# Performance work log

Measured on AMD Instinct MI355X. Metric: run time of the kernel, lower is better.

Reference implementation:

```python
import jax, jax.numpy as jnp
import numpy as np
import math

NLAT, NLON = 46, 90      # equiangular grid (in_shape == out_shape)
CH = 256                 # channels == kdim == vdim
BATCH = 1

def _cc_weights(n):
    # Clenshaw-Curtis quadrature weights (Waldvogel), nodes cos(k*pi/(n-1)); matches torch-harmonics equiangular grid
    n1 = n - 1
    N = np.arange(1, n1, 2)
    l = len(N)
    m = n1 - l
    v = np.concatenate([2.0 / N / (N - 2), [1.0 / N[-1]], np.zeros(m)])
    v = -v[:-1] - v[-1:0:-1]
    g0 = -np.ones(n1)
    g0[l] += n1
    g0[m] += n1
    g = g0 / (n1 ** 2 - 1 + (n1 % 2))
    w = np.fft.ifft(v + g).real
    return np.concatenate([w, w[:1]])

def _precompute_sparsity():
    # replicates _precompute_neighborhood_sparsity_s2: YZY-rotated north pole indicator within theta_cutoff
    lats = np.linspace(0.0, math.pi, NLAT)               # colatitudes of equiangular grid
    quad = (2.0 * math.pi / NLON) * _cc_weights(NLAT)    # per-latitude quadrature weights
    cutoff = math.pi / (NLAT - 1)                        # default theta_cutoff
    lons = np.linspace(0.0, 2.0 * math.pi, NLON + 1)[:-1]
    rows, cols = [], []
    for t in range(NLAT):
        a = -lats[t]
        beta = lons[None, :]
        gamma = lats[:, None]
        z = -np.cos(beta) * np.sin(a) * np.sin(gamma) + np.cos(a) * np.cos(gamma)
        x = np.cos(a) * np.cos(beta) * np.sin(gamma) + np.cos(gamma) * np.sin(a)
        y = np.sin(beta) * np.sin(gamma)
        nrm = np.sqrt(x * x + y * y + z * z)
        theta = np.arccos(np.clip(z / nrm, -1.0, 1.0))
        ii, jj = np.nonzero(theta <= cutoff)
        rows.append(np.full(ii.shape, t, dtype=np.int64))
        cols.append(ii * NLON + jj)
    row_ids = np.concatenate(rows).astype(np.int32)   # CSR row id per nnz (sorted)
    col_idx = np.concatenate(cols).astype(np.int32)   # flattened input index (at wo=0)
    return row_ids, col_idx, quad.astype(np.float32)

def setup_inputs() -> dict:
    key = jax.random.key(0)
    ks = jax.random.split(key, 9)
    row_ids, col_idx, quad = _precompute_sparsity()
    scale = 0.02  # sane init scale (module uses raw randn; trained weights would be O(this))
    return {
        "qo": jax.random.normal(ks[0], (BATCH, CH, NLAT, NLON), dtype=jnp.float32),
        "ki": jax.random.normal(ks[1], (BATCH, CH, NLAT, NLON), dtype=jnp.float32),
        "vi": jax.random.normal(ks[2], (BATCH, CH, NLAT, NLON), dtype=jnp.float32),
        "q_w": jax.random.normal(ks[3], (CH, CH), dtype=jnp.float32) * scale,
        "k_w": jax.random.normal(ks[4], (CH, CH), dtype=jnp.float32) * scale,
        "v_w": jax.random.normal(ks[5], (CH, CH), dtype=jnp.float32) * scale,
        "q_b": jax.random.normal(ks[6], (CH,), dtype=jnp.float32) * scale,
        "k_b": jax.random.normal(ks[7], (CH,), dtype=jnp.float32) * scale,
        "v_b": jax.random.normal(ks[8], (CH,), dtype=jnp.float32) * scale,
        "quad_w": jnp.asarray(quad),
        "row_ids": jnp.asarray(row_ids),
        "col_idx": jnp.asarray(col_idx),
    }

def reference(qo, ki, vi, q_w, k_w, v_w, q_b, k_b, v_b, quad_w, row_ids, col_idx):
    nlat, nlon = qo.shape[2], qo.shape[3]
    # 1x1 conv projections (F.conv2d with [out,in,1,1] kernels)
    q = jnp.einsum("kc,bchw->bkhw", q_w, qo) + q_b[None, :, None, None]
    k = jnp.einsum("kc,bchw->bkhw", k_w, ki) + k_b[None, :, None, None]
    v = jnp.einsum("vc,bchw->bvhw", v_w, vi) + v_b[None, :, None, None]

    hi = col_idx // nlon                                   # [N] input latitude per nnz
    wi0 = col_idx % nlon                                   # [N] input longitude at wo=0
    wo = jnp.arange(nlon)
    wi = (wi0[:, None] + wo[None, :]) % nlon               # [N, nlon] longitudes rotated by output lon

    kg = k[:, :, hi[:, None], wi]                          # [B, kdim, N, nlon] gathered keys
    qg = q[:, :, row_ids, :]                               # [B, kdim, N, nlon] query of owning output row
    qdotk = jnp.einsum("bcnw,bcnw->nbw", qg, kg)           # [N, B, nlon]

    # quadrature-weighted softmax over each output point's neighborhood (segment = output latitude row)
    seg_max = jax.ops.segment_max(qdotk, row_ids, num_segments=nlat, indices_are_sorted=True)
    seg_max = jax.lax.stop_gradient(seg_max)               # max shift cancels exactly in the ratio
    alpha = jnp.exp(qdotk - seg_max[row_ids]) * quad_w[hi][:, None, None]   # [N, B, nlon]
    denom = jax.ops.segment_sum(alpha, row_ids, num_segments=nlat, indices_are_sorted=True)  # [nlat, B, nlon]

    vg = jnp.transpose(v[:, :, hi[:, None], wi], (2, 0, 1, 3))   # [N, B, vdim, nlon]
    num = jax.ops.segment_sum(alpha[:, :, None, :] * vg, row_ids, num_segments=nlat, indices_are_sorted=True)
    out = num / denom[:, :, None, :]                       # [nlat, B, vdim, nlon]
    return jnp.transpose(out, (1, 2, 0, 3))                # [B, vdim, nlat, nlon]
```

## Files before the change

kernel.cpp:

```cpp
#include <hip/hip_runtime.h>
#include <math.h>

#define NLAT 46
#define NLON 90
#define CH   256
#define HW   (NLAT*NLON)
#define HWP  4160
#define HWT  32
#define NHT  130
#define XSTR 264

#define LIGHT_PER_XCD 473
#define SLOTS_PER_XCD (45 + LIGHT_PER_XCD)

typedef __attribute__((ext_vector_type(8))) short short8;
typedef __attribute__((ext_vector_type(4))) float floatx4;

__device__ __forceinline__ ushort f2bf(float f){
  uint u = __float_as_uint(f);
  u += 0x7fff + ((u >> 16) & 1);
  return (ushort)(u >> 16);
}
__device__ __forceinline__ float bf2f(ushort u){
  return __uint_as_float(((uint)u) << 16);
}

__device__ __forceinline__ int lower_bound_i(const int* __restrict__ a, int n, int key){
  int lo = 0, hi = n;
  while (lo < hi){ int mid = (lo + hi) >> 1; if (a[mid] < key) lo = mid + 1; else hi = mid; }
  return lo;
}

__global__ __launch_bounds__(256) void cast_w_kernel(
    const float* __restrict__ qw, const float* __restrict__ kw, const float* __restrict__ vw,
    ushort* __restrict__ Wq, ushort* __restrict__ Wk, ushort* __restrict__ Wv)
{
  const float* W; ushort* O;
  if (blockIdx.y == 0){ W = qw; O = Wq; }
  else if (blockIdx.y == 1){ W = kw; O = Wk; }
  else { W = vw; O = Wv; }
  for (int i = blockIdx.x * 256 + threadIdx.x; i < (CH*CH)/4; i += 8*256){
    float4 w = ((const float4*)W)[i];
    ushort4 o;
    o.x = f2bf(w.x); o.y = f2bf(w.y); o.z = f2bf(w.z); o.w = f2bf(w.w);
    ((ushort4*)O)[i] = o;
  }
}

__global__ __launch_bounds__(256) void fproj_kernel(
    const float* __restrict__ qo, const float* __restrict__ ki, const float* __restrict__ vi,
    const ushort* __restrict__ Wq, const ushort* __restrict__ Wk, const ushort* __restrict__ Wv,
    const float* __restrict__ qb, const float* __restrict__ kb, const float* __restrict__ vb,
    ushort* __restrict__ qP, ushort* __restrict__ kP, ushort* __restrict__ vP)
{
  const float* X; const ushort* Wb; const float* Bias; ushort* Out;
  if (blockIdx.y == 0){ X = qo; Wb = Wq; Bias = qb; Out = qP; }
  else if (blockIdx.y == 1){ X = ki; Wb = Wk; Bias = kb; Out = kP; }
  else { X = vi; Wb = Wv; Bias = vb; Out = vP; }

  __shared__ ushort Xs[HWT][XSTR];

  const int tid = threadIdx.x;
  const int hw0 = blockIdx.x * HWT;

  {
    int hwL = tid & 31;
    int cb  = tid >> 5;
    int hw  = hw0 + hwL;
    bool ok = hw < HW;
    const float* Xp = X + (size_t)(cb*32)*HW + (ok ? hw : 0);
    #pragma unroll
    for (int g = 0; g < 4; g++){
      short8 pk;
      #pragma unroll
      for (int u = 0; u < 8; u++){
        float f = ok ? Xp[(size_t)(g*8 + u)*HW] : 0.f;
        pk[u] = (short)f2bf(f);
      }
      *(short8*)(&Xs[hwL][cb*32 + g*8]) = pk;
    }
  }
  __syncthreads();

  const int lane = tid & 63;
  const int wave = tid >> 6;
  const int lm = lane & 15;
  const int lq = lane >> 4;
  const int kout_w = wave * 64;

  const ushort* Ap = Wb + (size_t)(kout_w + lm)*CH + lq*8;

  floatx4 acc[4][2];
  #pragma unroll
  for (int i = 0; i < 4; i++)
    #pragma unroll
    for (int j = 0; j < 2; j++) acc[i][j] = (floatx4){0,0,0,0};

  #pragma unroll
  for (int k0 = 0; k0 < 8; k0++){
    short8 a[4], b[2];
    #pragma unroll
    for (int i = 0; i < 4; i++)
      a[i] = *(const short8*)(Ap + (size_t)i*16*CH + k0*32);
    #pragma unroll
    for (int j = 0; j < 2; j++)
      b[j] = *(const short8*)(&Xs[j*16 + lm][lq*8 + k0*32]);
    #pragma unroll
    for (int i = 0; i < 4; i++)
      #pragma unroll
      for (int j = 0; j < 2; j++)
        acc[i][j] = __builtin_amdgcn_mfma_f32_16x16x32_bf16(a[i], b[j], acc[i][j], 0, 0, 0);
  }

  #pragma unroll
  for (int i = 0; i < 4; i++){
    int kout = kout_w + i*16 + lq*4;
    float4 bias = *(const float4*)(Bias + kout);
    #pragma unroll
    for (int j = 0; j < 2; j++){
      int hw = hw0 + j*16 + lm;
      if (hw < HW){
        ushort4 o;
        o.x = f2bf(acc[i][j][0] + bias.x);
        o.y = f2bf(acc[i][j][1] + bias.y);
        o.z = f2bf(acc[i][j][2] + bias.z);
        o.w = f2bf(acc[i][j][3] + bias.w);
        *(ushort4*)(Out + (size_t)hw*CH + kout) = o;
      }
    }
  }
}

__device__ __forceinline__ float4 ld_bf4(const ushort* p, int lane){
  ushort4 u = ((const ushort4*)p)[lane];
  float4 f;
  f.x = bf2f(u.x); f.y = bf2f(u.y); f.z = bf2f(u.z); f.w = bf2f(u.w);
  return f;
}

__global__ __launch_bounds__(256) void attn_kernel(
    const ushort* __restrict__ qP, const ushort* __restrict__ kP, const ushort* __restrict__ vP,
    const float* __restrict__ quad_w, const int* __restrict__ row_ids,
    const int* __restrict__ col_idx, int nnz, float* __restrict__ out)
{
  const int bid  = blockIdx.x;
  const int xcd  = bid & 7;
  const int slot = bid >> 3;

  int t, wo;
  if (slot < 45){
    int hu   = xcd * 45 + slot;
    int hidx = hu / 90;
    t  = (hidx < 2) ? hidx : 42 + hidx;
    wo = hu - hidx * 90;
  } else {
    int lu = xcd * LIGHT_PER_XCD + (slot - 45);
    if (lu >= 42 * NLON) return;
    int li = lu / NLON;
    t  = li + 2;
    wo = lu - li * NLON;
  }

  const int tid  = threadIdx.x;
  const int lane = tid & 63;
  const int wave = tid >> 6;

  const int start = lower_bound_i(row_ids, nnz, t);
  const int end   = lower_bound_i(row_ids, nnz, t + 1);

  const float4 qf = ld_bf4(qP + (size_t)(t * NLON + wo) * CH, lane);

  float denom = 0.f;
  float4 acc = make_float4(0.f, 0.f, 0.f, 0.f);

  int n = start + wave;
  for (; n + 4 < end; n += 8){
    int ciA = col_idx[n];
    int hiA = ciA / NLON;
    int wiA = ciA - hiA*NLON + wo; if (wiA >= NLON) wiA -= NLON;
    size_t offA = ((size_t)hiA*NLON + wiA) * CH;
    int ciB = col_idx[n + 4];
    int hiB = ciB / NLON;
    int wiB = ciB - hiB*NLON + wo; if (wiB >= NLON) wiB -= NLON;
    size_t offB = ((size_t)hiB*NLON + wiB) * CH;

    float4 kfA = ld_bf4(kP + offA, lane);
    float4 kfB = ld_bf4(kP + offB, lane);
    float sA = qf.x*kfA.x + qf.y*kfA.y + qf.z*kfA.z + qf.w*kfA.w;
    float sB = qf.x*kfB.x + qf.y*kfB.y + qf.z*kfB.z + qf.w*kfB.w;
    #pragma unroll
    for (int o = 32; o >= 1; o >>= 1){
      sA += __shfl_xor(sA, o, 64);
      sB += __shfl_xor(sB, o, 64);
    }
    float eA = __expf(sA) * quad_w[hiA];
    float eB = __expf(sB) * quad_w[hiB];
    float4 vfA = ld_bf4(vP + offA, lane);
    float4 vfB = ld_bf4(vP + offB, lane);
    denom += eA + eB;
    acc.x += eA*vfA.x + eB*vfB.x;
    acc.y += eA*vfA.y + eB*vfB.y;
    acc.z += eA*vfA.z + eB*vfB.z;
    acc.w += eA*vfA.w + eB*vfB.w;
  }
  if (n < end){
    int ci = col_idx[n];
    int hi = ci / NLON;
    int wi = ci - hi*NLON + wo; if (wi >= NLON) wi -= NLON;
    size_t off = ((size_t)hi*NLON + wi) * CH;
    float4 kf = ld_bf4(kP + off, lane);
    float s = qf.x*kf.x + qf.y*kf.y + qf.z*kf.z + qf.w*kf.w;
    #pragma unroll
    for (int o = 32; o >= 1; o >>= 1) s += __shfl_xor(s, o, 64);
    float e = __expf(s) * quad_w[hi];
    float4 vf = ld_bf4(vP + off, lane);
    denom += e;
    acc.x += e*vf.x; acc.y += e*vf.y; acc.z += e*vf.z; acc.w += e*vf.w;
  }

  __shared__ float sden[4];
  __shared__ float sacc[4][CH];
  if (lane == 0) sden[wave] = denom;
  sacc[wave][lane*4+0] = acc.x;
  sacc[wave][lane*4+1] = acc.y;
  sacc[wave][lane*4+2] = acc.z;
  sacc[wave][lane*4+3] = acc.w;
  __syncthreads();

  const float den = sden[0] + sden[1] + sden[2] + sden[3];
  const float num = sacc[0][tid] + sacc[1][tid] + sacc[2][tid] + sacc[3][tid];
  out[(size_t)tid * HW + t * NLON + wo] = num / den;
}

extern "C" void kernel_launch(void* const* d_in, const int* in_sizes, int n_in,
                              void* d_out, int out_size, void* d_ws, size_t ws_size,
                              hipStream_t stream)
{
  const float* qo   = (const float*)d_in[0];
  const float* ki   = (const float*)d_in[1];
  const float* vi   = (const float*)d_in[2];
  const float* qw   = (const float*)d_in[3];
  const float* kw   = (const float*)d_in[4];
  const float* vw   = (const float*)d_in[5];
  const float* qb   = (const float*)d_in[6];
  const float* kb   = (const float*)d_in[7];
  const float* vb   = (const float*)d_in[8];
  const float* quad = (const float*)d_in[9];
  const int* row_ids = (const int*)d_in[10];
  const int* col_idx = (const int*)d_in[11];
  const int nnz = in_sizes[10];

  ushort* ws = (ushort*)d_ws;
  const size_t TSZ = (size_t)HWP * CH;
  ushort* qP = ws;        ushort* kP = qP + TSZ;   ushort* vP = kP + TSZ;
  ushort* Wq = vP + TSZ;  ushort* Wk = Wq + CH*CH; ushort* Wv = Wk + CH*CH;

  cast_w_kernel<<<dim3(8, 3), 256, 0, stream>>>(qw, kw, vw, Wq, Wk, Wv);
  fproj_kernel<<<dim3(NHT, 3), 256, 0, stream>>>(qo, ki, vi, Wq, Wk, Wv, qb, kb, vb, qP, kP, vP);
  attn_kernel<<<dim3(8 * SLOTS_PER_XCD), 256, 0, stream>>>(qP, kP, vP, quad, row_ids, col_idx, nnz, (float*)d_out);
}
```

Measured before the change: 124.1 us.

## Fuse weight cast into projection and split attention waves into 16-lane groups

Drops the separate weight-cast kernel: the projection kernel now reads fp32 weights and converts them to bf16 in registers, which saves one launch but re-reads fp32 weights in every block. The attention kernel is restructured so each wave handles four neighbors at once, with each 16-lane group covering a full 256-channel row using 16-element vector loads. The dot-product reduction shrinks to a 4-step shuffle, and the cross-group accumulator reduction is deferred to the end. This raises register use per thread.

```diff
diff --git a/kernel.cpp b/kernel.cpp
--- a/kernel.cpp
+++ b/kernel.cpp
@@ -24,6 +24,9 @@
 __device__ __forceinline__ float bf2f(ushort u){
   return __uint_as_float(((uint)u) << 16);
 }
+__device__ __forceinline__ float bf2fs(short s){
+  return __uint_as_float(((uint)(ushort)s) << 16);
+}
 
 __device__ __forceinline__ int lower_bound_i(const int* __restrict__ a, int n, int key){
   int lo = 0, hi = n;
@@ -31,32 +34,16 @@
   return lo;
 }
 
-__global__ __launch_bounds__(256) void cast_w_kernel(
-    const float* __restrict__ qw, const float* __restrict__ kw, const float* __restrict__ vw,
-    ushort* __restrict__ Wq, ushort* __restrict__ Wk, ushort* __restrict__ Wv)
-{
-  const float* W; ushort* O;
-  if (blockIdx.y == 0){ W = qw; O = Wq; }
-  else if (blockIdx.y == 1){ W = kw; O = Wk; }
-  else { W = vw; O = Wv; }
-  for (int i = blockIdx.x * 256 + threadIdx.x; i < (CH*CH)/4; i += 8*256){
-    float4 w = ((const float4*)W)[i];
-    ushort4 o;
-    o.x = f2bf(w.x); o.y = f2bf(w.y); o.z = f2bf(w.z); o.w = f2bf(w.w);
-    ((ushort4*)O)[i] = o;
-  }
-}
-
 __global__ __launch_bounds__(256) void fproj_kernel(
     const float* __restrict__ qo, const float* __restrict__ ki, const float* __restrict__ vi,
-    const ushort* __restrict__ Wq, const ushort* __restrict__ Wk, const ushort* __restrict__ Wv,
+    const float* __restrict__ qw, const float* __restrict__ kw, const float* __restrict__ vw,
     const float* __restrict__ qb, const float* __restrict__ kb, const float* __restrict__ vb,
     ushort* __restrict__ qP, ushort* __restrict__ kP, ushort* __restrict__ vP)
 {
-  const float* X; const ushort* Wb; const float* Bias; ushort* Out;
-  if (blockIdx.y == 0){ X = qo; Wb = Wq; Bias = qb; Out = qP; }
-  else if (blockIdx.y == 1){ X = ki; Wb = Wk; Bias = kb; Out = kP; }
-  else { X = vi; Wb = Wv; Bias = vb; Out = vP; }
+  const float* X; const float* Wf; const float* Bias; ushort* Out;
+  if (blockIdx.y == 0){ X = qo; Wf = qw; Bias = qb; Out = qP; }
+  else if (blockIdx.y == 1){ X = ki; Wf = kw; Bias = kb; Out = kP; }
+  else { X = vi; Wf = vw; Bias = vb; Out = vP; }
 
   __shared__ ushort Xs[HWT][XSTR];
 
@@ -88,7 +75,7 @@
   const int lq = lane >> 4;
   const int kout_w = wave * 64;
 
-  const ushort* Ap = Wb + (size_t)(kout_w + lm)*CH + lq*8;
+  const float* Apf = Wf + (size_t)(kout_w + lm)*CH + lq*8;
 
   floatx4 acc[4][2];
   #pragma unroll
@@ -100,8 +87,15 @@
   for (int k0 = 0; k0 < 8; k0++){
     short8 a[4], b[2];
     #pragma unroll
-    for (int i = 0; i < 4; i++)
-      a[i] = *(const short8*)(Ap + (size_t)i*16*CH + k0*32);
+    for (int i = 0; i < 4; i++){
+      const float* p = Apf + (size_t)i*16*CH + k0*32;
+      float4 w0 = *(const float4*)p;
+      float4 w1 = *(const float4*)(p + 4);
+      a[i][0] = (short)f2bf(w0.x); a[i][1] = (short)f2bf(w0.y);
+      a[i][2] = (short)f2bf(w0.z); a[i][3] = (short)f2bf(w0.w);
+      a[i][4] = (short)f2bf(w1.x); a[i][5] = (short)f2bf(w1.y);
+      a[i][6] = (short)f2bf(w1.z); a[i][7] = (short)f2bf(w1.w);
+    }
     #pragma unroll
     for (int j = 0; j < 2; j++)
       b[j] = *(const short8*)(&Xs[j*16 + lm][lq*8 + k0*32]);
@@ -129,13 +123,6 @@
       }
     }
   }
-}
-
-__device__ __forceinline__ float4 ld_bf4(const ushort* p, int lane){
-  ushort4 u = ((const ushort4*)p)[lane];
-  float4 f;
-  f.x = bf2f(u.x); f.y = bf2f(u.y); f.z = bf2f(u.z); f.w = bf2f(u.w);
-  return f;
 }
 
 __global__ __launch_bounds__(256) void attn_kernel(
@@ -164,72 +151,76 @@
   const int tid  = threadIdx.x;
   const int lane = tid & 63;
   const int wave = tid >> 6;
+  const int g    = lane >> 4;
+  const int gl   = lane & 15;
 
   const int start = lower_bound_i(row_ids, nnz, t);
   const int end   = lower_bound_i(row_ids, nnz, t + 1);
 
-  const float4 qf = ld_bf4(qP + (size_t)(t * NLON + wo) * CH, lane);
-
-  float denom = 0.f;
-  float4 acc = make_float4(0.f, 0.f, 0.f, 0.f);
-
-  int n = start + wave;
-  for (; n + 4 < end; n += 8){
-    int ciA = col_idx[n];
-    int hiA = ciA / NLON;
-    int wiA = ciA - hiA*NLON + wo; if (wiA >= NLON) wiA -= NLON;
-    size_t offA = ((size_t)hiA*NLON + wiA) * CH;
-    int ciB = col_idx[n + 4];
-    int hiB = ciB / NLON;
-    int wiB = ciB - hiB*NLON + wo; if (wiB >= NLON) wiB -= NLON;
-    size_t offB = ((size_t)hiB*NLON + wiB) * CH;
-
-    float4 kfA = ld_bf4(kP + offA, lane);
-    float4 kfB = ld_bf4(kP + offB, lane);
-    float sA = qf.x*kfA.x + qf.y*kfA.y + qf.z*kfA.z + qf.w*kfA.w;
-    float sB = qf.x*kfB.x + qf.y*kfB.y + qf.z*kfB.z + qf.w*kfB.w;
-    #pragma unroll
-    for (int o = 32; o >= 1; o >>= 1){
-      sA += __shfl_xor(sA, o, 64);
-      sB += __shfl_xor(sB, o, 64);
-    }
-    float eA = __expf(sA) * quad_w[hiA];
-    float eB = __expf(sB) * quad_w[hiB];
-    float4 vfA = ld_bf4(vP + offA, lane);
-    float4 vfB = ld_bf4(vP + offB, lane);
-    denom += eA + eB;
-    acc.x += eA*vfA.x + eB*vfB.x;
-    acc.y += eA*vfA.y + eB*vfB.y;
-    acc.z += eA*vfA.z + eB*vfB.z;
-    acc.w += eA*vfA.w + eB*vfB.w;
-  }
-  if (n < end){
-    int ci = col_idx[n];
+  float qf[16];
+  {
+    const ushort* qrow = qP + (size_t)(t * NLON + wo) * CH + gl*16;
+    short8 q0 = *(const short8*)(qrow);
+    short8 q1 = *(const short8*)(qrow + 8);
+    #pragma unroll
+    for (int u = 0; u < 8; u++){ qf[u] = bf2fs(q0[u]); qf[8+u] = bf2fs(q1[u]); }
+  }
+
+  float den = 0.f;
+  float acc[16];
+  #pragma unroll
+  for (int u = 0; u < 16; u++) acc[u] = 0.f;
+
+  for (int n0 = start + wave*4 + g; n0 < end; n0 += 16){
+    int ci = col_idx[n0];
     int hi = ci / NLON;
     int wi = ci - hi*NLON + wo; if (wi >= NLON) wi -= NLON;
-    size_t off = ((size_t)hi*NLON + wi) * CH;
-    float4 kf = ld_bf4(kP + off, lane);
-    float s = qf.x*kf.x + qf.y*kf.y + qf.z*kf.z + qf.w*kf.w;
-    #pragma unroll
-    for (int o = 32; o >= 1; o >>= 1) s += __shfl_xor(s, o, 64);
+    size_t off = ((size_t)hi*NLON + wi) * CH + gl*16;
+
+    const short8* kp8 = (const short8*)(kP + off);
+    short8 k0 = kp8[0], k1 = kp8[1];
+    float s = 0.f;
+    #pragma unroll
+    for (int u = 0; u < 8; u++){
+      s += qf[u]   * bf2fs(k0[u]);
+      s += qf[8+u] * bf2fs(k1[u]);
+    }
+    s += __shfl_xor(s, 1, 64);
+    s += __shfl_xor(s, 2, 64);
+    s += __shfl_xor(s, 4, 64);
+    s += __shfl_xor(s, 8, 64);
+
     float e = __expf(s) * quad_w[hi];
-    float4 vf = ld_bf4(vP + off, lane);
-    denom += e;
-    acc.x += e*vf.x; acc.y += e*vf.y; acc.z += e*vf.z; acc.w += e*vf.w;
-  }
+    const short8* vp8 = (const short8*)(vP + off);
+    short8 v0 = vp8[0], v1 = vp8[1];
+    den += e;
+    #pragma unroll
+    for (int u = 0; u < 8; u++){
+      acc[u]   += e * bf2fs(v0[u]);
+      acc[8+u] += e * bf2fs(v1[u]);
+    }
+  }
+
+  #pragma unroll
+  for (int u = 0; u < 16; u++){
+    acc[u] += __shfl_xor(acc[u], 16, 64);
+    acc[u] += __shfl_xor(acc[u], 32, 64);
+  }
+  den += __shfl_xor(den, 16, 64);
+  den += __shfl_xor(den, 32, 64);
 
   __shared__ float sden[4];
   __shared__ float sacc[4][CH];
-  if (lane == 0) sden[wave] = denom;
-  sacc[wave][lane*4+0] = acc.x;
-  sacc[wave][lane*4+1] = acc.y;
-  sacc[wave][lane*4+2] = acc.z;
-  sacc[wave][lane*4+3] = acc.w;
+  if (lane == 0) sden[wave] = den;
+  if (g == 0){
+    #pragma unroll
+    for (int u = 0; u < 16; u++) sacc[wave][gl*16 + u] = acc[u];
+  }
   __syncthreads();
 
-  const float den = sden[0] + sden[1] + sden[2] + sden[3];
+  const float D   = sden[0] + sden[1] + sden[2] + sden[3];
   const float num = sacc[0][tid] + sacc[1][tid] + sacc[2][tid] + sacc[3][tid];
-  out[(size_t)tid * HW + t * NLON + wo] = num / den;
+  out[(size_t)tid * HW + t * NLON + wo] = num / D;
 }
 
 extern "C" void kernel_launch(void* const* d_in, const int* in_sizes, int n_in,
@@ -252,10 +243,8 @@
 
   ushort* ws = (ushort*)d_ws;
   const size_t TSZ = (size_t)HWP * CH;
-  ushort* qP = ws;        ushort* kP = qP + TSZ;   ushort* vP = kP + TSZ;
-  ushort* Wq = vP + TSZ;  ushort* Wk = Wq + CH*CH; ushort* Wv = Wk + CH*CH;
-
-  cast_w_kernel<<<dim3(8, 3), 256, 0, stream>>>(qw, kw, vw, Wq, Wk, Wv);
-  fproj_kernel<<<dim3(NHT, 3), 256, 0, stream>>>(qo, ki, vi, Wq, Wk, Wv, qb, kb, vb, qP, kP, vP);
+  ushort* qP = ws;  ushort* kP = qP + TSZ;  ushort* vP = kP + TSZ;
+
+  fproj_kernel<<<dim3(NHT, 3), 256, 0, stream>>>(qo, ki, vi, qw, kw, vw, qb, kb, vb, qP, kP, vP);
   attn_kernel<<<dim3(8 * SLOTS_PER_XCD), 256, 0, stream>>>(qP, kP, vP, quad, row_ids, col_idx, nnz, (float*)d_out);
 }
```

Result: faster. 121.1 us (-2.5%).
